# Performance work log

Hardware: AMD Instinct MI355X
Metric: run time of the kernel (lower is better)

## Reference

```python
import jax, jax.numpy as jnp
import numpy as np

N_NODES = 50000
N_EDGES = 1_600_000
IN_DIM = 256
OUT_DIM = 128
NEG_SLOPE = 0.01  # F.leaky_relu default


def setup_inputs() -> dict:
    key = jax.random.key(0)
    k1, k2, k3, k4, k5 = jax.random.split(key, 5)
    x = jax.random.normal(k1, (N_NODES, IN_DIM), dtype=jnp.float32)
    # glorot_init: uniform in [-r, r], r = sqrt(6/(in+out))
    r = np.sqrt(6.0 / (IN_DIM + OUT_DIM)).astype(np.float32)
    weight = jax.random.uniform(k2, (IN_DIM, OUT_DIM), dtype=jnp.float32, minval=-r, maxval=r)
    adj_rows = jax.random.randint(k3, (N_EDGES,), 0, N_NODES, dtype=jnp.int64 if jax.config.jax_enable_x64 else jnp.int32)
    adj_cols = jax.random.randint(k4, (N_EDGES,), 0, N_NODES, dtype=jnp.int64 if jax.config.jax_enable_x64 else jnp.int32)
    adj_vals = jax.random.uniform(k5, (N_EDGES,), dtype=jnp.float32)
    return {"x": x, "weight": weight, "adj_vals": adj_vals,
            "adj_rows": adj_rows, "adj_cols": adj_cols}


def reference(x, weight, adj_vals, adj_rows, adj_cols):
    # h = X @ W : [N, OUT_DIM]
    h = x @ weight
    # sparse adj @ h via edge-list SpMM: out[r] += v * h[c]
    msgs = adj_vals[:, None] * h[adj_cols]            # [E, OUT_DIM]
    agg = jax.ops.segment_sum(msgs, adj_rows, num_segments=N_NODES)
    # leaky_relu epilogue
    return jnp.where(agg >= 0, agg, NEG_SLOPE * agg)
```

## Files before the change

kernel.cpp:

```cpp
#include <hip/hip_runtime.h>
#include <hip/hip_fp16.h>

#define N_NODES 50000
#define N_EDGES 1600000
#define IN_DIM 256
#define OUT_DIM 128
#define NEG_SLOPE 0.01f

#define SB_SH     10
#define SB_ROWS   1024
#define NSB       ((N_NODES + SB_ROWS - 1) / SB_ROWS)
#define SEG       208

#define BIN_SH    5
#define BIN_ROWS  32
#define NBIN      ((N_NODES + BIN_ROWS - 1) / BIN_ROWS)
#define NBIN_PAD  (NSB * 32)
#define NPART     8
#define CAPB_TOT  (NPART * SEG)
#define OVF_CAP   65536

#define SCAT_BLOCKS 256
#define CONVW_BLOCKS 8
#define EPB_S (N_EDGES / SCAT_BLOCKS)
#define SCAT_ITERS ((EPB_S + 511) / 512)

typedef _Float16 f16x8 __attribute__((ext_vector_type(8)));
typedef float    f32x4 __attribute__((ext_vector_type(4)));
typedef float    f32x8 __attribute__((ext_vector_type(8)));

__device__ __forceinline__ float lrelu(float v) {
    return v >= 0.f ? v : NEG_SLOPE * v;
}

#define BM 128
#define GEMM_BLOCKS ((N_NODES + BM - 1) / BM)

#define CVT16(lo, hi) do { \
    lo[0]=(_Float16)xr[0].x; lo[1]=(_Float16)xr[0].y; lo[2]=(_Float16)xr[0].z; lo[3]=(_Float16)xr[0].w; \
    lo[4]=(_Float16)xr[1].x; lo[5]=(_Float16)xr[1].y; lo[6]=(_Float16)xr[1].z; lo[7]=(_Float16)xr[1].w; \
    hi[0]=(_Float16)xr[2].x; hi[1]=(_Float16)xr[2].y; hi[2]=(_Float16)xr[2].z; hi[3]=(_Float16)xr[2].w; \
    hi[4]=(_Float16)xr[3].x; hi[5]=(_Float16)xr[3].y; hi[6]=(_Float16)xr[3].z; hi[7]=(_Float16)xr[3].w; \
} while (0)

__global__ __launch_bounds__(256, 2) void gemm_xw_mfma(const float* __restrict__ x,
                                                       const __half* __restrict__ wtl,
                                                       __half* __restrict__ h) {
    __shared__ f16x8 wt8[32 * 128];
    __shared__ f16x8 xs8[2][4][BM];

    const int t    = threadIdx.x;
    const int lane = t & 63;
    const int wv   = t >> 6;
    const int row0 = blockIdx.x * BM;

    {
        const int4* src = (const int4*)wtl;
        int4* dst = (int4*)wt8;
#pragma unroll
        for (int i = 0; i < 16; ++i) dst[i * 256 + t] = src[i * 256 + t];
    }

    const int srow = t >> 1;
    const int skh  = t & 1;
    const int grow = row0 + srow;
    const bool rv  = grow < N_NODES;
    const float* xp = x + (size_t)(rv ? grow : 0) * IN_DIM + skh * 16;

    float4 xr[4];
#pragma unroll
    for (int i = 0; i < 4; ++i)
        xr[i] = rv ? ((const float4*)xp)[i] : make_float4(0.f, 0.f, 0.f, 0.f);
    {
        f16x8 lo, hi;
        CVT16(lo, hi);
        xs8[0][skh * 2 + 0][srow] = lo;
        xs8[0][skh * 2 + 1][srow] = hi;
    }
    __syncthreads();

    f32x4 acc[2][8];
#pragma unroll
    for (int mf = 0; mf < 2; ++mf)
#pragma unroll
        for (int nf = 0; nf < 8; ++nf) acc[mf][nf] = (f32x4){0.f, 0.f, 0.f, 0.f};

    const int kg  = lane >> 4;
    const int l15 = lane & 15;
    const int mb  = (wv << 5) + l15;

#pragma unroll
    for (int ks = 0; ks < 8; ++ks) {
        const int cur = ks & 1;
        if (ks < 7) {
#pragma unroll
            for (int i = 0; i < 4; ++i)
                xr[i] = rv ? ((const float4*)(xp + (ks + 1) * 32))[i]
                           : make_float4(0.f, 0.f, 0.f, 0.f);
        }
        const f16x8 b0 = xs8[cur][kg][mb];
        const f16x8 b1 = xs8[cur][kg][mb + 16];
#pragma unroll
        for (int nf = 0; nf < 8; ++nf) {
            const f16x8 a = wt8[(((ks << 2) | kg) << 7) + (nf << 4) + l15];
            acc[0][nf] = __builtin_amdgcn_mfma_f32_16x16x32_f16(a, b0, acc[0][nf], 0, 0, 0);
            acc[1][nf] = __builtin_amdgcn_mfma_f32_16x16x32_f16(a, b1, acc[1][nf], 0, 0, 0);
        }
        if (ks < 7) {
            f16x8 lo, hi;
            CVT16(lo, hi);
            xs8[cur ^ 1][skh * 2 + 0][srow] = lo;
            xs8[cur ^ 1][skh * 2 + 1][srow] = hi;
            __syncthreads();
        }
    }

    const int rg = lane >> 4;
#pragma unroll
    for (int mf = 0; mf < 2; ++mf) {
        const int m = row0 + (wv << 5) + (mf << 4) + l15;
        if (m < N_NODES) {
            __half* hp = h + (size_t)m * OUT_DIM + (rg << 2);
#pragma unroll
            for (int nf = 0; nf < 8; ++nf) {
                union { ushort4 u; __half f[4]; } o;
                o.f[0] = __float2half(acc[mf][nf][0]);
                o.f[1] = __float2half(acc[mf][nf][1]);
                o.f[2] = __float2half(acc[mf][nf][2]);
                o.f[3] = __float2half(acc[mf][nf][3]);
                *(ushort4*)(hp + (nf << 4)) = o.u;
            }
        }
    }
}

__global__ __launch_bounds__(512) void scatter_coarse(const int* __restrict__ rows,
                                                      const int* __restrict__ cols,
                                                      const float* __restrict__ vals,
                                                      int* __restrict__ ccnt,
                                                      int* __restrict__ ovfcnt,
                                                      int2* __restrict__ cbuf,
                                                      int2* __restrict__ ovfbuf,
                                                      const float* __restrict__ w,
                                                      __half* __restrict__ wtl) {
    if (blockIdx.x >= SCAT_BLOCKS) {
        const int e0 = ((blockIdx.x - SCAT_BLOCKS) * 512 + threadIdx.x) * 8;
        const int k  = e0 >> 7;
        const int n0 = e0 & 127;
        const float4 a = *(const float4*)(w + e0);
        const float4 b = *(const float4*)(w + e0 + 4);
        __half* dst = wtl + ((size_t)((k >> 3) * 128 + n0)) * 8 + (k & 7);
        dst[0]  = __float2half(a.x);
        dst[8]  = __float2half(a.y);
        dst[16] = __float2half(a.z);
        dst[24] = __float2half(a.w);
        dst[32] = __float2half(b.x);
        dst[40] = __float2half(b.y);
        dst[48] = __float2half(b.z);
        dst[56] = __float2half(b.w);
        return;
    }

    __shared__ int2 lsort[EPB_S];
    __shared__ int  hist[NSB];
    __shared__ int  cstart[NSB];

    const int t    = threadIdx.x;
    const int lane = t & 63;
    const int blk  = blockIdx.x;
    const int ebase = blk * EPB_S;

    if (t < NSB) hist[t] = 0;
    __syncthreads();

    int myr[SCAT_ITERS];
#pragma unroll
    for (int k = 0; k < SCAT_ITERS; ++k) {
        const int i = k * 512 + t;
        myr[k] = -1;
        if (i < EPB_S) {
            myr[k] = rows[ebase + i];
            atomicAdd(&hist[myr[k] >> SB_SH], 1);
        }
    }
    __syncthreads();

    if (t < 64) {
        const int v = (t < NSB) ? hist[t] : 0;
        int s = v;
#pragma unroll
        for (int off = 1; off < 64; off <<= 1) {
            const int u = __shfl_up(s, off);
            if (lane >= off) s += u;
        }
        if (t < NSB) { cstart[t] = s - v; hist[t] = s - v; }
    }
    __syncthreads();

#pragma unroll
    for (int k = 0; k < SCAT_ITERS; ++k) {
        const int i = k * 512 + t;
        if (i < EPB_S) {
            const int e = ebase + i;
            const int r = myr[k];
            const int pos = atomicAdd(&hist[r >> SB_SH], 1);
            lsort[pos] = make_int2((int)(((unsigned)r << 16) | (unsigned)cols[e]),
                                   __float_as_int(vals[e]));
        }
    }
    __syncthreads();

    for (int i = t; i < EPB_S; i += 512) {
        const int2 rc = lsort[i];
        const int sb  = (int)(((unsigned)rc.x) >> 16) >> SB_SH;
        const int off = i - cstart[sb];
        if (off < SEG) {
            cbuf[((size_t)sb * SCAT_BLOCKS + blk) * SEG + off] = rc;
        } else {
            const int p = atomicAdd(ovfcnt, 1);
            if (p < OVF_CAP) ovfbuf[p] = rc;
        }
    }
    __syncthreads();

    if (t < NSB) ccnt[t * SCAT_BLOCKS + blk] = min(hist[t] - cstart[t], SEG);
}

__global__ __launch_bounds__(512) void scatter_fine(const int* __restrict__ ccnt,
                                                    int* __restrict__ fcnt,
                                                    int* __restrict__ ovfcnt,
                                                    const int2* __restrict__ cbuf,
                                                    int2* __restrict__ ebuf,
                                                    int2* __restrict__ ovfbuf) {
    __shared__ int2 lsort[32 * SEG];
    __shared__ int  hist[32];
    __shared__ int  cstart[32];
    __shared__ int  scnt[32];
    __shared__ int  stot;

    const int t    = threadIdx.x;
    const int lane = t & 63;
    const int wv   = t >> 6;
    const int sb   = blockIdx.x / NPART;
    const int p    = blockIdx.x % NPART;

    if (t < 32) {
        hist[t] = 0;
        scnt[t] = ccnt[sb * SCAT_BLOCKS + p * 32 + t];
    }
    __syncthreads();

    for (int j = 0; j < 4; ++j) {
        const int seg = (wv << 2) + j;
        const int cnt = scnt[seg];
        const size_t sbase = ((size_t)sb * SCAT_BLOCKS + p * 32 + seg) * SEG;
        for (int i = lane; i < cnt; i += 64)
            atomicAdd(&hist[(cbuf[sbase + i].x >> 21) & 31], 1);
    }
    __syncthreads();

    if (t < 32) {
        const int v = hist[t];
        int s = v;
#pragma unroll
        for (int off = 1; off < 32; off <<= 1) {
            const int u = __shfl_up(s, off);
            if (t >= off) s += u;
        }
        if (t == 31) stot = s;
        cstart[t] = s - v;
        hist[t]   = s - v;
    }
    __syncthreads();

    for (int j = 0; j < 4; ++j) {
        const int seg = (wv << 2) + j;
        const int cnt = scnt[seg];
        const size_t sbase = ((size_t)sb * SCAT_BLOCKS + p * 32 + seg) * SEG;
        for (int i = lane; i < cnt; i += 64) {
            const int2 rc = cbuf[sbase + i];
            const unsigned urow = ((unsigned)rc.x) >> 16;
            const int fb = (int)((urow >> BIN_SH) & 31);
            const int pos = atomicAdd(&hist[fb], 1);
            lsort[pos] = make_int2((rc.x & 0xFFFF) | (int)((urow & (BIN_ROWS - 1)) << 16)
                                                   | (fb << 21), rc.y);
        }
    }
    __syncthreads();

    const int tot = stot;
    for (int i = t; i < tot; i += 512) {
        const int2 rc = lsort[i];
        const int fb  = (rc.x >> 21) & 31;
        const int off = i - cstart[fb];
        if (off < SEG) {
            ebuf[(((size_t)sb * 32 + fb) * NPART + p) * SEG + off] = rc;
        } else {
            const int q = atomicAdd(ovfcnt, 1);
            if (q < OVF_CAP) {
                const int row = (sb << SB_SH) | (fb << BIN_SH) | ((rc.x >> 16) & 31);
                ovfbuf[q] = make_int2((int)(((unsigned)row << 16) | (unsigned)(rc.x & 0xFFFF)), rc.y);
            }
        }
    }
    __syncthreads();

    if (t < 32) fcnt[((sb * 32 + t) * NPART) + p] = min(hist[t] - cstart[t], SEG);
}

#define NCLS 256

#define STAGE(IT, HV, VV) do {                                                  \
    _Pragma("unroll")                                                           \
    for (int q = 0; q < 4; ++q) {                                               \
        const int idx = beg[q] + ((IT) << 2) + grp;                             \
        const bool vld = idx < end[q];                                          \
        const int2 r = srec[vld ? idx : last];                                  \
        VV[q] = vld ? __int_as_float(r.y) : 0.f;                                \
        HV[q] = *(const f16x8*)(h + (size_t)(r.x & 0xFFFF) * OUT_DIM + (gl << 3)); \
    }                                                                           \
} while (0)

__global__ __launch_bounds__(512, 4) void sort_gather(const int* __restrict__ fcnt,
                                                      const int* __restrict__ ovfcnt,
                                                      const int2* __restrict__ ebuf,
                                                      const int2* __restrict__ ovfbuf,
                                                      const __half* __restrict__ h,
                                                      float* __restrict__ out) {
    __shared__ int2 urec[CAPB_TOT];
    __shared__ int2 srec[CAPB_TOT];
    __shared__ int  hist[NCLS];
    __shared__ int  pfx[NCLS];
    __shared__ int  rowoff_l[BIN_ROWS + 1];
    __shared__ int  wsum[4];
    __shared__ int  poff[NPART + 1];

    const int t    = threadIdx.x;
    const int bin  = blockIdx.x;
    const int wv   = t >> 6;
    const int lane = t & 63;

    if (t < NCLS) hist[t] = 0;
    if (t == 0) {
        int a = 0;
        poff[0] = 0;
#pragma unroll
        for (int p = 0; p < NPART; ++p) { a += fcnt[bin * NPART + p]; poff[p + 1] = a; }
    }
    __syncthreads();
    const int cnt = poff[NPART];

    {
        const int cp = poff[wv + 1] - poff[wv];
        const size_t pb = ((size_t)bin * NPART + wv) * SEG;
        const int ub = poff[wv];
        for (int i = lane; i < cp; i += 64) {
            const int2 r = ebuf[pb + i];
            urec[ub + i] = r;
            atomicAdd(&hist[(((r.x >> 16) & 31) << 3) | ((r.x & 0xFFFF) >> 13)], 1);
        }
    }
    __syncthreads();

    {
        const int v = (t < NCLS) ? hist[t] : 0;
        int s = v;
#pragma unroll
        for (int off = 1; off < 64; off <<= 1) {
            const int u = __shfl_up(s, off);
            if (lane >= off) s += u;
        }
        if (t < NCLS && lane == 63) wsum[wv] = s;
        __syncthreads();
        if (t == 0) {
            int a = 0;
#pragma unroll
            for (int i = 0; i < 4; ++i) { const int c = wsum[i]; wsum[i] = a; a += c; }
        }
        __syncthreads();
        if (t < NCLS) {
            const int incl = s + wsum[wv];
            pfx[t]  = incl;
            hist[t] = incl - v;
        }
    }
    __syncthreads();
    if (t < BIN_ROWS) rowoff_l[t] = t ? pfx[(t << 3) - 1] : 0;
    if (t == BIN_ROWS) rowoff_l[BIN_ROWS] = cnt;
    __syncthreads();

    for (int i = t; i < cnt; i += 512) {
        const int2 r = urec[i];
        const int cls = (((r.x >> 16) & 31) << 3) | ((r.x & 0xFFFF) >> 13);
        const int pos = atomicAdd(&hist[cls], 1);
        srec[pos] = r;
    }
    __syncthreads();

    const int grp = lane >> 4;
    const int gl  = lane & 15;
    const int r0  = wv << 2;
    const int last = cnt > 0 ? cnt - 1 : 0;

    int beg[4], end[4];
#pragma unroll
    for (int q = 0; q < 4; ++q) { beg[q] = rowoff_l[r0 + q]; end[q] = rowoff_l[r0 + q + 1]; }
    int nmax = 0;
#pragma unroll
    for (int q = 0; q < 4; ++q) nmax = max(nmax, end[q] - beg[q]);
    const int iters = (nmax + 3) >> 2;

    f32x8 acc[4];
#pragma unroll
    for (int q = 0; q < 4; ++q) acc[q] = (f32x8){0.f,0.f,0.f,0.f,0.f,0.f,0.f,0.f};

    if (cnt > 0 && iters > 0) {
        f16x8 hc[4], hn[4];
        float vc[4], vn[4];
        STAGE(0, hc, vc);
        for (int it = 0; it < iters; ++it) {
            const int itn = (it + 1 < iters) ? it + 1 : it;
            STAGE(itn, hn, vn);
            __builtin_amdgcn_sched_barrier(0);
#pragma unroll
            for (int q = 0; q < 4; ++q)
#pragma unroll
                for (int j = 0; j < 8; ++j) acc[q][j] += vc[q] * (float)hc[q][j];
            __builtin_amdgcn_sched_barrier(0);
#pragma unroll
            for (int q = 0; q < 4; ++q) { hc[q] = hn[q]; vc[q] = vn[q]; }
        }
    }

    int novf = *ovfcnt;
    if (novf > OVF_CAP) novf = OVF_CAP;
    for (int e = 0; e < novf; ++e) {
        const int2 rec = ovfbuf[e];
        const unsigned urow = ((unsigned)rec.x) >> 16;
        if ((int)(urow >> BIN_SH) == bin && grp == 0) {
            const int lr = (int)(urow & (BIN_ROWS - 1)) - r0;
            if (lr >= 0 && lr < 4) {
                const float v = __int_as_float(rec.y);
                const f16x8 hv = *(const f16x8*)(h + (size_t)(rec.x & 0xFFFF) * OUT_DIM + (gl << 3));
#pragma unroll
                for (int q = 0; q < 4; ++q)
                    if (q == lr)
#pragma unroll
                        for (int j = 0; j < 8; ++j) acc[q][j] += v * (float)hv[j];
            }
        }
    }

#pragma unroll
    for (int q = 0; q < 4; ++q)
#pragma unroll
        for (int j = 0; j < 8; ++j) {
            float x = acc[q][j];
            x += __shfl_xor(x, 16);
            x += __shfl_xor(x, 32);
            acc[q][j] = x;
        }

    float res[8];
#pragma unroll
    for (int j = 0; j < 8; ++j) {
        float x = acc[0][j];
        x = (grp == 1) ? acc[1][j] : x;
        x = (grp == 2) ? acc[2][j] : x;
        x = (grp == 3) ? acc[3][j] : x;
        res[j] = lrelu(x);
    }
    const int grow = (bin << BIN_SH) + r0 + grp;
    if (grow < N_NODES) {
        float* op = out + (size_t)grow * OUT_DIM + (gl << 3);
        *(float4*)op       = make_float4(res[0], res[1], res[2], res[3]);
        *(float4*)(op + 4) = make_float4(res[4], res[5], res[6], res[7]);
    }
}

extern "C" void kernel_launch(void* const* d_in, const int* in_sizes, int n_in,
                              void* d_out, int out_size, void* d_ws, size_t ws_size,
                              hipStream_t stream) {
    const float* x    = (const float*)d_in[0];
    const float* w    = (const float*)d_in[1];
    const float* vals = (const float*)d_in[2];
    const int*   rows = (const int*)d_in[3];
    const int*   cols = (const int*)d_in[4];
    float* out = (float*)d_out;

    char* ws = (char*)d_ws;
    size_t off = 0;
    auto alloc = [&](size_t bytes) {
        void* p = ws + off;
        off = (off + bytes + 255) & ~(size_t)255;
        return p;
    };
    int2*  cbuf    = (int2*) alloc((size_t)NSB * SCAT_BLOCKS * SEG * sizeof(int2));
    __half* h      = (__half*)cbuf;
    int2*  ebuf    = (int2*) alloc((size_t)NBIN_PAD * NPART * SEG * sizeof(int2));
    int2*  ovfbuf  = (int2*) alloc((size_t)OVF_CAP * sizeof(int2));
    __half* wtl    = (__half*)alloc((size_t)IN_DIM * OUT_DIM * sizeof(__half));
    int*   ccnt    = (int*)  alloc((size_t)NSB * SCAT_BLOCKS * sizeof(int));
    int*   fcnt    = (int*)  alloc((size_t)NBIN_PAD * NPART * sizeof(int));
    int*   ovfcnt  = (int*)  alloc(sizeof(int));

    hipMemsetAsync(ovfcnt, 0, sizeof(int), stream);

    scatter_coarse<<<SCAT_BLOCKS + CONVW_BLOCKS, 512, 0, stream>>>(rows, cols, vals,
                                                                   ccnt, ovfcnt, cbuf, ovfbuf, w, wtl);
    scatter_fine<<<NSB * NPART, 512, 0, stream>>>(ccnt, fcnt, ovfcnt, cbuf, ebuf, ovfbuf);
    gemm_xw_mfma<<<GEMM_BLOCKS, 256, 0, stream>>>(x, wtl, h);
    sort_gather<<<NBIN, 512, 0, stream>>>(fcnt, ovfcnt, ebuf, ovfbuf, h, out);
}
```

Before: 203.8 us.

## Fuse coarse scatter and GEMM into one prep kernel with compact segment buffers

Merges the coarse edge-bucketing pass, the weight fp16 conversion, the X@W MFMA GEMM and the overflow-counter reset into a single prep launch. This removes the memset and one kernel launch and lets the GEMM overlap with the scatter. Coarse buckets are now written as contiguous per-block sorted runs with a start-offset table, and fine buckets as contiguous per-partition runs with start/count arrays. That replaces the fixed padded SEG slots and changes where records spill to overflow. In exchange, every GEMM block converts W to fp16 itself in two halves with extra syncs, and only half the threads of the 512-thread block do GEMM work.

```diff
diff --git a/kernel.cpp b/kernel.cpp
--- a/kernel.cpp
+++ b/kernel.cpp
@@ -8,22 +8,23 @@
 #define NEG_SLOPE 0.01f
 
 #define SB_SH     10
-#define SB_ROWS   1024
-#define NSB       ((N_NODES + SB_ROWS - 1) / SB_ROWS)
-#define SEG       208
-
+#define NSB       49
 #define BIN_SH    5
 #define BIN_ROWS  32
-#define NBIN      ((N_NODES + BIN_ROWS - 1) / BIN_ROWS)
 #define NBIN_PAD  (NSB * 32)
 #define NPART     8
-#define CAPB_TOT  (NPART * SEG)
+#define ECAP      4608
+#define SEGP      256
+#define CAPG      (NPART * SEGP)
 #define OVF_CAP   65536
 
 #define SCAT_BLOCKS 256
-#define CONVW_BLOCKS 8
 #define EPB_S (N_EDGES / SCAT_BLOCKS)
 #define SCAT_ITERS ((EPB_S + 511) / 512)
+
+#define BM 128
+#define GEMM_BLOCKS ((N_NODES + BM - 1) / BM)
+#define PREP_BLOCKS (SCAT_BLOCKS + GEMM_BLOCKS + 1)
 
 typedef _Float16 f16x8 __attribute__((ext_vector_type(8)));
 typedef float    f32x4 __attribute__((ext_vector_type(4)));
@@ -32,9 +33,6 @@
 __device__ __forceinline__ float lrelu(float v) {
     return v >= 0.f ? v : NEG_SLOPE * v;
 }
-
-#define BM 128
-#define GEMM_BLOCKS ((N_NODES + BM - 1) / BM)
 
 #define CVT16(lo, hi) do { \
     lo[0]=(_Float16)xr[0].x; lo[1]=(_Float16)xr[0].y; lo[2]=(_Float16)xr[0].z; lo[3]=(_Float16)xr[0].w; \
@@ -43,39 +41,104 @@
     hi[4]=(_Float16)xr[3].x; hi[5]=(_Float16)xr[3].y; hi[6]=(_Float16)xr[3].z; hi[7]=(_Float16)xr[3].w; \
 } while (0)
 
-__global__ __launch_bounds__(256, 2) void gemm_xw_mfma(const float* __restrict__ x,
-                                                       const __half* __restrict__ wtl,
-                                                       __half* __restrict__ h) {
-    __shared__ f16x8 wt8[32 * 128];
-    __shared__ f16x8 xs8[2][4][BM];
-
-    const int t    = threadIdx.x;
+__global__ __launch_bounds__(512, 2) void prep(const int* __restrict__ rows,
+                                               const int* __restrict__ cols,
+                                               const float* __restrict__ vals,
+                                               const float* __restrict__ x,
+                                               const float* __restrict__ w,
+                                               int* __restrict__ cstartarr,
+                                               int* __restrict__ ovfcnt,
+                                               int2* __restrict__ cbuf,
+                                               __half* __restrict__ h) {
+    __shared__ __attribute__((aligned(16))) char smem[50432];
+    const int bid = blockIdx.x;
+    const int t   = threadIdx.x;
+
+    if (bid >= SCAT_BLOCKS + GEMM_BLOCKS) {
+        if (t == 0) *ovfcnt = 0;
+        return;
+    }
+
+    if (bid < SCAT_BLOCKS) {
+        int2* lsort  = (int2*)smem;
+        int*  hist   = (int*)(smem + 50000);
+        int*  cstart = (int*)(smem + 50200);
+        const int lane  = t & 63;
+        const int blk   = bid;
+        const int ebase = blk * EPB_S;
+
+        if (t < NSB) hist[t] = 0;
+        __syncthreads();
+
+        int myr[SCAT_ITERS];
+#pragma unroll
+        for (int k = 0; k < SCAT_ITERS; ++k) {
+            const int i = k * 512 + t;
+            myr[k] = -1;
+            if (i < EPB_S) {
+                myr[k] = rows[ebase + i];
+                atomicAdd(&hist[myr[k] >> SB_SH], 1);
+            }
+        }
+        __syncthreads();
+
+        if (t < 64) {
+            const int v = (t < NSB) ? hist[t] : 0;
+            int s = v;
+#pragma unroll
+            for (int off = 1; off < 64; off <<= 1) {
+                const int u = __shfl_up(s, off);
+                if (lane >= off) s += u;
+            }
+            if (t < NSB) { cstart[t] = s - v; hist[t] = s - v; }
+        }
+        __syncthreads();
+
+#pragma unroll
+        for (int k = 0; k < SCAT_ITERS; ++k) {
+            const int i = k * 512 + t;
+            if (i < EPB_S) {
+                const int e = ebase + i;
+                const int r = myr[k];
+                const int pos = atomicAdd(&hist[r >> SB_SH], 1);
+                lsort[pos] = make_int2((int)(((unsigned)r << 16) | (unsigned)cols[e]),
+                                       __float_as_int(vals[e]));
+            }
+        }
+        __syncthreads();
+
+        {
+            const int4* src = (const int4*)lsort;
+            int4* dst = (int4*)(cbuf + (size_t)blk * EPB_S);
+            for (int i = t; i < EPB_S / 2; i += 512) dst[i] = src[i];
+        }
+        if (t < NSB)  cstartarr[blk * 50 + t]   = cstart[t];
+        if (t == NSB) cstartarr[blk * 50 + NSB] = EPB_S;
+        return;
+    }
+
+    f16x8* wt8h = (f16x8*)smem;
+    f16x8* xs8  = (f16x8*)(smem + 32768);
+    const int a256 = (t < 256);
     const int lane = t & 63;
     const int wv   = t >> 6;
-    const int row0 = blockIdx.x * BM;
-
-    {
-        const int4* src = (const int4*)wtl;
-        int4* dst = (int4*)wt8;
-#pragma unroll
-        for (int i = 0; i < 16; ++i) dst[i * 256 + t] = src[i * 256 + t];
-    }
+    const int row0 = (bid - SCAT_BLOCKS) * BM;
 
     const int srow = t >> 1;
     const int skh  = t & 1;
     const int grow = row0 + srow;
-    const bool rv  = grow < N_NODES;
+    const bool rv  = a256 && (grow < N_NODES);
     const float* xp = x + (size_t)(rv ? grow : 0) * IN_DIM + skh * 16;
 
     float4 xr[4];
-#pragma unroll
-    for (int i = 0; i < 4; ++i)
-        xr[i] = rv ? ((const float4*)xp)[i] : make_float4(0.f, 0.f, 0.f, 0.f);
-    {
+    if (a256) {
+#pragma unroll
+        for (int i = 0; i < 4; ++i)
+            xr[i] = rv ? ((const float4*)xp)[i] : make_float4(0.f, 0.f, 0.f, 0.f);
         f16x8 lo, hi;
         CVT16(lo, hi);
-        xs8[0][skh * 2 + 0][srow] = lo;
-        xs8[0][skh * 2 + 1][srow] = hi;
+        xs8[(0 * 4 + skh * 2 + 0) * 128 + srow] = lo;
+        xs8[(0 * 4 + skh * 2 + 1) * 128 + srow] = hi;
     }
     __syncthreads();
 
@@ -85,157 +148,95 @@
 #pragma unroll
         for (int nf = 0; nf < 8; ++nf) acc[mf][nf] = (f32x4){0.f, 0.f, 0.f, 0.f};
 
-    const int kg  = lane >> 4;
+    const int kgl = lane >> 4;
     const int l15 = lane & 15;
     const int mb  = (wv << 5) + l15;
 
 #pragma unroll
-    for (int ks = 0; ks < 8; ++ks) {
-        const int cur = ks & 1;
-        if (ks < 7) {
-#pragma unroll
-            for (int i = 0; i < 4; ++i)
-                xr[i] = rv ? ((const float4*)(xp + (ks + 1) * 32))[i]
-                           : make_float4(0.f, 0.f, 0.f, 0.f);
-        }
-        const f16x8 b0 = xs8[cur][kg][mb];
-        const f16x8 b1 = xs8[cur][kg][mb + 16];
-#pragma unroll
-        for (int nf = 0; nf < 8; ++nf) {
-            const f16x8 a = wt8[(((ks << 2) | kg) << 7) + (nf << 4) + l15];
-            acc[0][nf] = __builtin_amdgcn_mfma_f32_16x16x32_f16(a, b0, acc[0][nf], 0, 0, 0);
-            acc[1][nf] = __builtin_amdgcn_mfma_f32_16x16x32_f16(a, b1, acc[1][nf], 0, 0, 0);
-        }
-        if (ks < 7) {
-            f16x8 lo, hi;
-            CVT16(lo, hi);
-            xs8[cur ^ 1][skh * 2 + 0][srow] = lo;
-            xs8[cur ^ 1][skh * 2 + 1][srow] = hi;
+    for (int H = 0; H < 2; ++H) {
+        if (a256) {
+#pragma unroll
+            for (int itr = 0; itr < 8; ++itr) {
+                const int e  = itr * 2048 + t * 8;
+                const int kl = e >> 7;
+                const int n0 = e & 127;
+                const float4 a4 = *(const float4*)(w + (size_t)((H << 7) + kl) * 128 + n0);
+                const float4 b4 = *(const float4*)(w + (size_t)((H << 7) + kl) * 128 + n0 + 4);
+                __half* d = (__half*)wt8h + (size_t)(((kl >> 3) << 7) + n0) * 8 + (kl & 7);
+                d[0]  = __float2half(a4.x);
+                d[8]  = __float2half(a4.y);
+                d[16] = __float2half(a4.z);
+                d[24] = __float2half(a4.w);
+                d[32] = __float2half(b4.x);
+                d[40] = __float2half(b4.y);
+                d[48] = __float2half(b4.z);
+                d[56] = __float2half(b4.w);
+            }
+        }
+        __syncthreads();
+
+#pragma unroll
+        for (int ksl = 0; ksl < 4; ++ksl) {
+            const int ks  = H * 4 + ksl;
+            const int cur = ks & 1;
+            if (a256 && ks < 7) {
+#pragma unroll
+                for (int i = 0; i < 4; ++i)
+                    xr[i] = rv ? ((const float4*)(xp + (ks + 1) * 32))[i]
+                               : make_float4(0.f, 0.f, 0.f, 0.f);
+            }
+            if (a256) {
+                const f16x8 b0 = xs8[(cur * 4 + kgl) * 128 + mb];
+                const f16x8 b1 = xs8[(cur * 4 + kgl) * 128 + mb + 16];
+                const int abase = ((ksl * 4 + kgl) << 7) + l15;
+#pragma unroll
+                for (int nf = 0; nf < 8; ++nf) {
+                    const f16x8 a = wt8h[abase + (nf << 4)];
+                    acc[0][nf] = __builtin_amdgcn_mfma_f32_16x16x32_f16(a, b0, acc[0][nf], 0, 0, 0);
+                    acc[1][nf] = __builtin_amdgcn_mfma_f32_16x16x32_f16(a, b1, acc[1][nf], 0, 0, 0);
+                }
+            }
+            if (a256 && ks < 7) {
+                f16x8 lo, hi;
+                CVT16(lo, hi);
+                xs8[((cur ^ 1) * 4 + skh * 2 + 0) * 128 + srow] = lo;
+                xs8[((cur ^ 1) * 4 + skh * 2 + 1) * 128 + srow] = hi;
+            }
             __syncthreads();
         }
     }
 
-    const int rg = lane >> 4;
-#pragma unroll
-    for (int mf = 0; mf < 2; ++mf) {
-        const int m = row0 + (wv << 5) + (mf << 4) + l15;
-        if (m < N_NODES) {
-            __half* hp = h + (size_t)m * OUT_DIM + (rg << 2);
-#pragma unroll
-            for (int nf = 0; nf < 8; ++nf) {
-                union { ushort4 u; __half f[4]; } o;
-                o.f[0] = __float2half(acc[mf][nf][0]);
-                o.f[1] = __float2half(acc[mf][nf][1]);
-                o.f[2] = __float2half(acc[mf][nf][2]);
-                o.f[3] = __float2half(acc[mf][nf][3]);
-                *(ushort4*)(hp + (nf << 4)) = o.u;
+    if (a256) {
+        const int rg = lane >> 4;
+#pragma unroll
+        for (int mf = 0; mf < 2; ++mf) {
+            const int m = row0 + (wv << 5) + (mf << 4) + l15;
+            if (m < N_NODES) {
+                __half* hp = h + (size_t)m * OUT_DIM + (rg << 2);
+#pragma unroll
+                for (int nf = 0; nf < 8; ++nf) {
+                    union { ushort4 u; __half f[4]; } o;
+                    o.f[0] = __float2half(acc[mf][nf][0]);
+                    o.f[1] = __float2half(acc[mf][nf][1]);
+                    o.f[2] = __float2half(acc[mf][nf][2]);
+                    o.f[3] = __float2half(acc[mf][nf][3]);
+                    *(ushort4*)(hp + (nf << 4)) = o.u;
+                }
             }
         }
     }
 }
 
-__global__ __launch_bounds__(512) void scatter_coarse(const int* __restrict__ rows,
-                                                      const int* __restrict__ cols,
-                                                      const float* __restrict__ vals,
-                                                      int* __restrict__ ccnt,
-                                                      int* __restrict__ ovfcnt,
-                                                      int2* __restrict__ cbuf,
-                                                      int2* __restrict__ ovfbuf,
-                                                      const float* __restrict__ w,
-                                                      __half* __restrict__ wtl) {
-    if (blockIdx.x >= SCAT_BLOCKS) {
-        const int e0 = ((blockIdx.x - SCAT_BLOCKS) * 512 + threadIdx.x) * 8;
-        const int k  = e0 >> 7;
-        const int n0 = e0 & 127;
-        const float4 a = *(const float4*)(w + e0);
-        const float4 b = *(const float4*)(w + e0 + 4);
-        __half* dst = wtl + ((size_t)((k >> 3) * 128 + n0)) * 8 + (k & 7);
-        dst[0]  = __float2half(a.x);
-        dst[8]  = __float2half(a.y);
-        dst[16] = __float2half(a.z);
-        dst[24] = __float2half(a.w);
-        dst[32] = __float2half(b.x);
-        dst[40] = __float2half(b.y);
-        dst[48] = __float2half(b.z);
-        dst[56] = __float2half(b.w);
-        return;
-    }
-
-    __shared__ int2 lsort[EPB_S];
-    __shared__ int  hist[NSB];
-    __shared__ int  cstart[NSB];
-
-    const int t    = threadIdx.x;
-    const int lane = t & 63;
-    const int blk  = blockIdx.x;
-    const int ebase = blk * EPB_S;
-
-    if (t < NSB) hist[t] = 0;
-    __syncthreads();
-
-    int myr[SCAT_ITERS];
-#pragma unroll
-    for (int k = 0; k < SCAT_ITERS; ++k) {
-        const int i = k * 512 + t;
-        myr[k] = -1;
-        if (i < EPB_S) {
-            myr[k] = rows[ebase + i];
-            atomicAdd(&hist[myr[k] >> SB_SH], 1);
-        }
-    }
-    __syncthreads();
-
-    if (t < 64) {
-        const int v = (t < NSB) ? hist[t] : 0;
-        int s = v;
-#pragma unroll
-        for (int off = 1; off < 64; off <<= 1) {
-            const int u = __shfl_up(s, off);
-            if (lane >= off) s += u;
-        }
-        if (t < NSB) { cstart[t] = s - v; hist[t] = s - v; }
-    }
-    __syncthreads();
-
-#pragma unroll
-    for (int k = 0; k < SCAT_ITERS; ++k) {
-        const int i = k * 512 + t;
-        if (i < EPB_S) {
-            const int e = ebase + i;
-            const int r = myr[k];
-            const int pos = atomicAdd(&hist[r >> SB_SH], 1);
-            lsort[pos] = make_int2((int)(((unsigned)r << 16) | (unsigned)cols[e]),
-                                   __float_as_int(vals[e]));
-        }
-    }
-    __syncthreads();
-
-    for (int i = t; i < EPB_S; i += 512) {
-        const int2 rc = lsort[i];
-        const int sb  = (int)(((unsigned)rc.x) >> 16) >> SB_SH;
-        const int off = i - cstart[sb];
-        if (off < SEG) {
-            cbuf[((size_t)sb * SCAT_BLOCKS + blk) * SEG + off] = rc;
-        } else {
-            const int p = atomicAdd(ovfcnt, 1);
-            if (p < OVF_CAP) ovfbuf[p] = rc;
-        }
-    }
-    __syncthreads();
-
-    if (t < NSB) ccnt[t * SCAT_BLOCKS + blk] = min(hist[t] - cstart[t], SEG);
-}
-
-__global__ __launch_bounds__(512) void scatter_fine(const int* __restrict__ ccnt,
-                                                    int* __restrict__ fcnt,
+__global__ __launch_bounds__(512) void scatter_fine(const int* __restrict__ cstartarr,
+                                                    int* __restrict__ fs,
+                                                    int* __restrict__ fc,
                                                     int* __restrict__ ovfcnt,
                                                     const int2* __restrict__ cbuf,
                                                     int2* __restrict__ ebuf,
                                                     int2* __restrict__ ovfbuf) {
-    __shared__ int2 lsort[32 * SEG];
-    __shared__ int  hist[32];
-    __shared__ int  cstart[32];
-    __shared__ int  scnt[32];
+    __shared__ int2 lsort[ECAP];
+    __shared__ int  hist[32], cstart[32], fcv[32];
+    __shared__ int  scnt[32], sstart[32];
     __shared__ int  stot;
 
     const int t    = threadIdx.x;
@@ -245,17 +246,21 @@
     const int p    = blockIdx.x % NPART;
 
     if (t < 32) {
-        hist[t] = 0;
-        scnt[t] = ccnt[sb * SCAT_BLOCKS + p * 32 + t];
+        const int blk = p * 32 + t;
+        const int s0 = cstartarr[blk * 50 + sb];
+        const int s1 = cstartarr[blk * 50 + sb + 1];
+        scnt[t]   = s1 - s0;
+        sstart[t] = blk * EPB_S + s0;
+        hist[t]   = 0;
     }
     __syncthreads();
 
     for (int j = 0; j < 4; ++j) {
-        const int seg = (wv << 2) + j;
-        const int cnt = scnt[seg];
-        const size_t sbase = ((size_t)sb * SCAT_BLOCKS + p * 32 + seg) * SEG;
-        for (int i = lane; i < cnt; i += 64)
-            atomicAdd(&hist[(cbuf[sbase + i].x >> 21) & 31], 1);
+        const int s = (wv << 2) + j;
+        const int c = scnt[s];
+        const int base = sstart[s];
+        for (int i = lane; i < c; i += 64)
+            atomicAdd(&hist[(cbuf[base + i].x >> 21) & 31], 1);
     }
     __syncthreads();
 
@@ -274,28 +279,42 @@
     __syncthreads();
 
     for (int j = 0; j < 4; ++j) {
-        const int seg = (wv << 2) + j;
-        const int cnt = scnt[seg];
-        const size_t sbase = ((size_t)sb * SCAT_BLOCKS + p * 32 + seg) * SEG;
-        for (int i = lane; i < cnt; i += 64) {
-            const int2 rc = cbuf[sbase + i];
-            const unsigned urow = ((unsigned)rc.x) >> 16;
-            const int fb = (int)((urow >> BIN_SH) & 31);
+        const int s = (wv << 2) + j;
+        const int c = scnt[s];
+        const int base = sstart[s];
+        for (int i = lane; i < c; i += 64) {
+            const int2 rc = cbuf[base + i];
+            const int fb = (rc.x >> 21) & 31;
             const int pos = atomicAdd(&hist[fb], 1);
-            lsort[pos] = make_int2((rc.x & 0xFFFF) | (int)((urow & (BIN_ROWS - 1)) << 16)
-                                                   | (fb << 21), rc.y);
-        }
-    }
-    __syncthreads();
-
-    const int tot = stot;
+            const int lrow = (rc.x >> 16) & 31;
+            if (pos < ECAP) {
+                lsort[pos] = make_int2((rc.x & 0xFFFF) | (lrow << 16) | (fb << 21), rc.y);
+            } else {
+                const int q = atomicAdd(ovfcnt, 1);
+                if (q < OVF_CAP) ovfbuf[q] = rc;
+            }
+        }
+    }
+    __syncthreads();
+
+    if (t < 32) {
+        int c = hist[t] - cstart[t];
+        if (c > SEGP) c = SEGP;
+        if (cstart[t] + c > ECAP) c = (cstart[t] < ECAP) ? (ECAP - cstart[t]) : 0;
+        fcv[t] = c;
+        fs[(sb * 32 + t) * NPART + p] = cstart[t];
+        fc[(sb * 32 + t) * NPART + p] = c;
+    }
+    __syncthreads();
+
+    const int tot = min(stot, ECAP);
+    int2* dst = ebuf + (size_t)(sb * NPART + p) * ECAP;
     for (int i = t; i < tot; i += 512) {
         const int2 rc = lsort[i];
+        dst[i] = rc;
         const int fb  = (rc.x >> 21) & 31;
         const int off = i - cstart[fb];
-        if (off < SEG) {
-            ebuf[(((size_t)sb * 32 + fb) * NPART + p) * SEG + off] = rc;
-        } else {
+        if (off >= fcv[fb]) {
             const int q = atomicAdd(ovfcnt, 1);
             if (q < OVF_CAP) {
                 const int row = (sb << SB_SH) | (fb << BIN_SH) | ((rc.x >> 16) & 31);
@@ -303,9 +322,6 @@
             }
         }
     }
-    __syncthreads();
-
-    if (t < 32) fcnt[((sb * 32 + t) * NPART) + p] = min(hist[t] - cstart[t], SEG);
 }
 
 #define NCLS 256
@@ -321,41 +337,45 @@
     }                                                                           \
 } while (0)
 
-__global__ __launch_bounds__(512, 4) void sort_gather(const int* __restrict__ fcnt,
+__global__ __launch_bounds__(512, 4) void sort_gather(const int* __restrict__ fs,
+                                                      const int* __restrict__ fc,
                                                       const int* __restrict__ ovfcnt,
                                                       const int2* __restrict__ ebuf,
                                                       const int2* __restrict__ ovfbuf,
                                                       const __half* __restrict__ h,
                                                       float* __restrict__ out) {
-    __shared__ int2 urec[CAPB_TOT];
-    __shared__ int2 srec[CAPB_TOT];
+    __shared__ int2 urec[CAPG];
+    __shared__ int2 srec[CAPG];
     __shared__ int  hist[NCLS];
     __shared__ int  pfx[NCLS];
     __shared__ int  rowoff_l[BIN_ROWS + 1];
     __shared__ int  wsum[4];
     __shared__ int  poff[NPART + 1];
+    __shared__ int  fsrt[NPART];
 
     const int t    = threadIdx.x;
     const int bin  = blockIdx.x;
     const int wv   = t >> 6;
     const int lane = t & 63;
+    const int sb   = bin >> 5;
 
     if (t < NCLS) hist[t] = 0;
+    if (t < NPART) fsrt[t] = fs[bin * NPART + t];
     if (t == 0) {
         int a = 0;
         poff[0] = 0;
 #pragma unroll
-        for (int p = 0; p < NPART; ++p) { a += fcnt[bin * NPART + p]; poff[p + 1] = a; }
+        for (int p = 0; p < NPART; ++p) { a += fc[bin * NPART + p]; poff[p + 1] = a; }
     }
     __syncthreads();
     const int cnt = poff[NPART];
 
     {
         const int cp = poff[wv + 1] - poff[wv];
-        const size_t pb = ((size_t)bin * NPART + wv) * SEG;
+        const int2* src = ebuf + (size_t)(sb * NPART + wv) * ECAP + fsrt[wv];
         const int ub = poff[wv];
         for (int i = lane; i < cp; i += 64) {
-            const int2 r = ebuf[pb + i];
+            const int2 r = src[i];
             urec[ub + i] = r;
             atomicAdd(&hist[(((r.x >> 16) & 31) << 3) | ((r.x & 0xFFFF) >> 13)], 1);
         }
@@ -495,20 +515,18 @@
         off = (off + bytes + 255) & ~(size_t)255;
         return p;
     };
-    int2*  cbuf    = (int2*) alloc((size_t)NSB * SCAT_BLOCKS * SEG * sizeof(int2));
-    __half* h      = (__half*)cbuf;
-    int2*  ebuf    = (int2*) alloc((size_t)NBIN_PAD * NPART * SEG * sizeof(int2));
-    int2*  ovfbuf  = (int2*) alloc((size_t)OVF_CAP * sizeof(int2));
-    __half* wtl    = (__half*)alloc((size_t)IN_DIM * OUT_DIM * sizeof(__half));
-    int*   ccnt    = (int*)  alloc((size_t)NSB * SCAT_BLOCKS * sizeof(int));
-    int*   fcnt    = (int*)  alloc((size_t)NBIN_PAD * NPART * sizeof(int));
-    int*   ovfcnt  = (int*)  alloc(sizeof(int));
-
-    hipMemsetAsync(ovfcnt, 0, sizeof(int), stream);
-
-    scatter_coarse<<<SCAT_BLOCKS + CONVW_BLOCKS, 512, 0, stream>>>(rows, cols, vals,
-                                                                   ccnt, ovfcnt, cbuf, ovfbuf, w, wtl);
-    scatter_fine<<<NSB * NPART, 512, 0, stream>>>(ccnt, fcnt, ovfcnt, cbuf, ebuf, ovfbuf);
-    gemm_xw_mfma<<<GEMM_BLOCKS, 256, 0, stream>>>(x, wtl, h);
-    sort_gather<<<NBIN, 512, 0, stream>>>(fcnt, ovfcnt, ebuf, ovfbuf, h, out);
+    int2*   cbuf     = (int2*)  alloc((size_t)N_EDGES * sizeof(int2));
+    __half* h        = (__half*)alloc((size_t)N_NODES * OUT_DIM * sizeof(__half));
+    int2*   ebuf     = (int2*)  alloc((size_t)NSB * NPART * ECAP * sizeof(int2));
+    int2*   ovfbuf   = (int2*)  alloc((size_t)OVF_CAP * sizeof(int2));
+    int*    cstartarr= (int*)   alloc((size_t)SCAT_BLOCKS * 50 * sizeof(int));
+    int*    fs       = (int*)   alloc((size_t)NBIN_PAD * NPART * sizeof(int));
+    int*    fc       = (int*)   alloc((size_t)NBIN_PAD * NPART * sizeof(int));
+    int*    ovfcnt   = (int*)   alloc(sizeof(int));
+
+    prep<<<PREP_BLOCKS, 512, 0, stream>>>(rows, cols, vals, x, w,
+                                          cstartarr, ovfcnt, cbuf, h);
+    scatter_fine<<<NSB * NPART, 512, 0, stream>>>(cstartarr, fs, fc, ovfcnt,
+                                                  cbuf, ebuf, ovfbuf);
+    sort_gather<<<NBIN_PAD, 512, 0, stream>>>(fs, fc, ovfcnt, ebuf, ovfbuf, h, out);
 }
```

After: 202.7 us. About the same (-0.5%).
